# Kernel tuning notes

Measured on AMD Instinct MI355X. Metric: run time of the kernel, lower is better.

## Reference

```python
import jax, jax.numpy as jnp
import numpy as np
import math

D_EMBED = 128   # per-head dim (config.d_embed)
N_HEADS = 12
ROPE_BASE = 10000.0


def rope(x):
    # x: [B, H, S, D]; interleaved-pair rotary embedding on last dim
    B, H, S, D = x.shape
    half = D // 2
    inv_freq = 1.0 / (ROPE_BASE ** (jnp.arange(0, half, dtype=jnp.float32) * 2.0 / D))
    ang = jnp.arange(S, dtype=jnp.float32)[:, None] * inv_freq[None, :]  # [S, D/2]
    cos, sin = jnp.cos(ang), jnp.sin(ang)
    xp = x.reshape(B, H, S, half, 2)
    x1, x2 = xp[..., 0], xp[..., 1]
    o1 = x1 * cos - x2 * sin
    o2 = x1 * sin + x2 * cos
    return jnp.stack([o1, o2], axis=-1).reshape(B, H, S, D)


def setup_inputs() -> dict:
    key = jax.random.key(0)
    ks = jax.random.split(key, 5)
    B, S, E = 2, 2048, D_EMBED // 2
    inner = N_HEADS * D_EMBED
    sc = 0.02
    return {
        "q": jax.random.normal(ks[0], (B, S, E), dtype=jnp.float32),
        "Wq": jax.random.normal(ks[1], (inner, E), dtype=jnp.float32) * sc,
        "Wk": jax.random.normal(ks[2], (inner, E), dtype=jnp.float32) * sc,
        "Wv": jax.random.normal(ks[3], (inner, E), dtype=jnp.float32) * sc,
        "Wo": jax.random.normal(ks[4], (E, inner), dtype=jnp.float32) * sc,
    }


def reference(q, Wq, Wk, Wv, Wo):
    B, S, E = q.shape
    H, D = N_HEADS, D_EMBED
    scale = 1.0 / math.sqrt(D)

    def proj(x, W):
        return (x @ W.T).reshape(B, S, H, D).transpose(0, 2, 1, 3)  # [B,H,S,D]

    qh = rope(proj(q, Wq))
    kh = rope(proj(q, Wk))
    vh = proj(q, Wv)

    scores = jnp.einsum("bhsd,bhtd->bhst", qh, kh) * scale  # [B,H,S,S]
    causal = jnp.tril(jnp.ones((S, S), dtype=bool))
    scores = jnp.where(causal, scores, -jnp.inf)
    probs = jax.nn.softmax(scores, axis=-1)  # dropout omitted (eval mode)
    out = jnp.einsum("bhst,bhtd->bhsd", probs, vh)
    out = out.transpose(0, 2, 1, 3).reshape(B, S, H * D)
    return out @ Wo.T  # [B,S,E]
```

## Files before the change

### kernel.cpp

```cpp
#include <hip/hip_runtime.h>
#include <stdint.h>


typedef short v8s __attribute__((ext_vector_type(8)));
typedef unsigned int v4u __attribute__((ext_vector_type(4)));
typedef float v4f __attribute__((ext_vector_type(4)));
typedef float v16f __attribute__((ext_vector_type(16)));

#define MFMA16(a, b, c) __builtin_amdgcn_mfma_f32_16x16x32_bf16(a, b, c, 0, 0, 0)
#define MFMA32(a, b, c) __builtin_amdgcn_mfma_f32_32x32x16_bf16(a, b, c, 0, 0, 0)

#if __has_builtin(__builtin_amdgcn_exp2f)
#define EXP2(x) __builtin_amdgcn_exp2f(x)
#else
#define EXP2(x) exp2f(x)
#endif

#define SCALE2 (0.08838834764831845f * 1.4426950408889634f)

__device__ __forceinline__ unsigned short f2bf(float f) {
  uint32_t u = __builtin_bit_cast(uint32_t, f);
  u += 0x7FFFu + ((u >> 16) & 1u);
  return (unsigned short)(u >> 16);
}

__device__ __forceinline__ uint32_t packbf(float lo, float hi) {
  return __builtin_amdgcn_perm(__builtin_bit_cast(uint32_t, hi) + 0x8000u,
                               __builtin_bit_cast(uint32_t, lo) + 0x8000u,
                               0x07060302u);
}

__device__ __forceinline__ v16f zero16() {
  v16f z;
#pragma unroll
  for (int i = 0; i < 16; ++i) z[i] = 0.f;
  return z;
}

__device__ __forceinline__ void gl_lds16(const unsigned short* g, unsigned short* l) {
  __builtin_amdgcn_global_load_lds(
      (const __attribute__((address_space(1))) uint32_t*)g,
      (__attribute__((address_space(3))) uint32_t*)l, 16, 0, 0);
}

__global__ __launch_bounds__(256) void rope_table(float* __restrict__ cos_t,
                                                  float* __restrict__ sin_t) {
  int idx = blockIdx.x * 256 + threadIdx.x;
  if (idx >= 2048 * 64) return;
  int s = idx >> 6, f = idx & 63;
  float inv = exp2f((float)f * -0.20762050593046014f);
  float ang = (float)s * inv;
  float si, co;
  sincosf(ang, &si, &co);
  cos_t[idx] = co;
  sin_t[idx] = si;
}

__global__ __launch_bounds__(256) void proj_rope(
    const float* __restrict__ x, const float* __restrict__ Wq,
    const float* __restrict__ Wk, const float* __restrict__ Wv,
    const float* __restrict__ cos_t, const float* __restrict__ sin_t,
    unsigned short* __restrict__ qh, unsigned short* __restrict__ kh,
    unsigned short* __restrict__ vt) {
  const int wave = threadIdx.x >> 6, lane = threadIdx.x & 63;
  const int l16 = lane & 15, quad = lane >> 4;
  const int by = blockIdx.y;
  const int o_base = by * 64 + wave * 16;
  const int mat = o_base / 1536;
  const int inner0 = o_base % 1536;
  const int d0w = inner0 & 127;
  const float* Wsrc = (mat == 0) ? Wq : ((mat == 1) ? Wk : Wv);
  const float qscale = (mat == 0) ? SCALE2 : 1.0f;

  __shared__ __align__(16) unsigned short Lt[64][72];

  v8s wb[2];
  {
    const float* wr = Wsrc + (size_t)(inner0 + l16) * 64 + quad * 8;
#pragma unroll
    for (int s = 0; s < 2; ++s) {
      float4 a = *(const float4*)(wr + s * 32);
      float4 b = *(const float4*)(wr + s * 32 + 4);
      v8s t;
      t[0] = (short)f2bf(a.x); t[1] = (short)f2bf(a.y);
      t[2] = (short)f2bf(a.z); t[3] = (short)f2bf(a.w);
      t[4] = (short)f2bf(b.x); t[5] = (short)f2bf(b.y);
      t[6] = (short)f2bf(b.z); t[7] = (short)f2bf(b.w);
      wb[s] = t;
    }
  }

  const int d = d0w + l16;
  const int half = d >> 1;

#pragma unroll
  for (int i = 0; i < 4; ++i) {
    const int tok0 = blockIdx.x * 64 + i * 16;
    const float* xr = x + (size_t)(tok0 + l16) * 64 + quad * 8;
    v8s xa[2];
#pragma unroll
    for (int s = 0; s < 2; ++s) {
      float4 a = *(const float4*)(xr + s * 32);
      float4 b = *(const float4*)(xr + s * 32 + 4);
      v8s t;
      t[0] = (short)f2bf(a.x); t[1] = (short)f2bf(a.y);
      t[2] = (short)f2bf(a.z); t[3] = (short)f2bf(a.w);
      t[4] = (short)f2bf(b.x); t[5] = (short)f2bf(b.y);
      t[6] = (short)f2bf(b.z); t[7] = (short)f2bf(b.w);
      xa[s] = t;
    }
    v4f acc = {0.f, 0.f, 0.f, 0.f};
    acc = MFMA16(xa[0], wb[0], acc);
    acc = MFMA16(xa[1], wb[1], acc);

    if (mat < 2) {
#pragma unroll
      for (int r = 0; r < 4; ++r) {
        int sidx = (tok0 + quad * 4 + r) & 2047;
        float val = acc[r];
        float prt = __shfl_xor(val, 1);
        float co = cos_t[sidx * 64 + half];
        float si = sin_t[sidx * 64 + half];
        float rot = ((d & 1) == 0) ? (val * co - prt * si)
                                   : (prt * si + val * co);
        Lt[i * 16 + quad * 4 + r][wave * 16 + l16] = f2bf(rot * qscale);
      }
    } else {
#pragma unroll
      for (int r = 0; r < 4; ++r)
        Lt[wave * 16 + l16][i * 16 + quad * 4 + r] = f2bf(acc[r]);
    }
  }
  __syncthreads();

  const int matb = (by * 64) / 1536;
  const int innerb = (by * 64) % 1536;
  const int hb = innerb >> 7;
  const int d0b = innerb & 127;
  const int b = (blockIdx.x * 64) >> 11;
  const int tokbase = (blockIdx.x * 64) & 2047;
#pragma unroll
  for (int jj = 0; jj < 2; ++jj) {
    int cid = jj * 256 + threadIdx.x;
    int outer = cid >> 3, ic = cid & 7;
    v8s val = *(const v8s*)&Lt[outer][ic * 8];
    if (matb < 2) {
      unsigned short* dst = (matb == 0 ? qh : kh) +
          (((size_t)(b * 12 + hb)) * 2048 + tokbase + outer) * 128 + d0b + ic * 8;
      *(v8s*)dst = val;
    } else {
      const int kt = tokbase >> 6;
      const int G = ic >> 1, hhb = ic & 1;
      const int dd = d0b + outer;
      unsigned short* dst = vt +
          ((((((size_t)(b * 12 + hb)) * 32 + kt) * 4 + G) * 4 + (dd >> 5)) * 64 +
           hhb * 32 + (dd & 31)) * 8;
      *(v8s*)dst = val;
    }
  }
}

__global__ __launch_bounds__(512, 2) void attn(
    const unsigned short* __restrict__ qh, const unsigned short* __restrict__ kh,
    const unsigned short* __restrict__ vtf, unsigned short* __restrict__ att,
    const float* __restrict__ Wo, unsigned short* __restrict__ wob) {
  extern __shared__ __align__(16) unsigned short SH[];
  unsigned short* KSH = SH;
  unsigned short* VSH = SH + 32768;

  const int n = blockIdx.x;
  int qb, bh;
  if (n < 240)      { qb = 15 - n / 24; bh = n % 24; }
  else if (n < 256) { qb = 5;           bh = n - 240; }
  else if (n < 376) { int r = n - 256; qb = r / 24; bh = r % 24; }
  else              { qb = 5;           bh = 16 + (n - 376); }

  const int t = threadIdx.x;
  const int lane = t & 63;
  const int l31 = lane & 31, hh = lane >> 5;
  const int w = t >> 6;
  const int rg = w & 3, kherd = w >> 2;
  const int r0w = qb * 128 + rg * 32;
  const int qrow = r0w + l31;
  const int rowmax = r0w + 31;

  const unsigned short* Qb = qh + (size_t)bh * 2048 * 128;
  const unsigned short* Kb = kh + (size_t)bh * 2048 * 128;
  const unsigned short* Vb = vtf + (size_t)bh * 262144;

  v8s qa[8];
  {
    const unsigned short* qr = Qb + (size_t)qrow * 128 + hh * 8;
#pragma unroll
    for (int ks = 0; ks < 8; ++ks) qa[ks] = *(const v8s*)(qr + ks * 16);
  }

  int offK[2];
#pragma unroll
  for (int i2 = 0; i2 < 2; ++i2) {
    int flat = i2 * 512 + t;
    int kr = flat >> 4, kc = flat & 15;
    offK[i2] = kr * 128 + ((kc ^ (kr & 15)) << 3);
  }
  auto stageK = [&](int ktile, int slot) {
    const unsigned short* kg = Kb + ((size_t)(ktile << 6)) * 128;
    unsigned short* db = &KSH[slot * 8192];
#pragma unroll
    for (int i2 = 0; i2 < 2; ++i2)
      gl_lds16(kg + offK[i2], db + ((i2 * 512 + t) << 3));
  };
  auto stageV = [&](int ktile, int slot) {
    const unsigned short* vg = Vb + (size_t)ktile * 8192;
    unsigned short* db = &VSH[slot * 8192];
#pragma unroll
    for (int i2 = 0; i2 < 2; ++i2)
      gl_lds16(vg + ((i2 * 512 + t) << 3), db + ((i2 * 512 + t) << 3));
  };

  v16f O[4];
#pragma unroll
  for (int i = 0; i < 4; ++i) O[i] = zero16();
  float lsum = 0.f;

  const int NS = qb + 1;
  stageK(0, 0); stageV(0, 0);
  stageK(qb + 1, 2); stageV(qb + 1, 2);
  asm volatile("s_waitcnt vmcnt(0)" ::: "memory");

  for (int i = 0; i < NS; ++i) {
    __builtin_amdgcn_s_barrier();
    __builtin_amdgcn_sched_barrier(0);
    const int kt = kherd ? (qb + 1 + i) : i;
    const int key0 = kt << 6;
    const bool active = key0 <= rowmax;
    const bool hi = (key0 + 32) <= rowmax;

    if (i + 1 < NS) {
      stageK(i + 1, (i + 1) & 1);
      stageV(i + 1, (i + 1) & 1);
      stageK(qb + 2 + i, 2 + ((i + 1) & 1));
      stageV(qb + 2 + i, 2 + ((i + 1) & 1));
    }
    __builtin_amdgcn_sched_barrier(0);

    if (active) {
      const unsigned short* Kl = &KSH[(kherd * 2 + (i & 1)) * 8192];
      const unsigned short* Vl = &VSH[(kherd * 2 + (i & 1)) * 8192];
      const bool mask0 = (key0 + 31) > r0w;
      const bool mask1 = (key0 + 63) > r0w;

      auto softpack = [&](const v16f& SS, const v16f& ST, int kh2, bool needmask,
                          uint32_t* W) {
#pragma unroll
        for (int m = 0; m < 8; ++m) {
          float pa = EXP2(SS[2 * m] + ST[2 * m]);
          float pb = EXP2(SS[2 * m + 1] + ST[2 * m + 1]);
          if (needmask) {
            int keyb = key0 + kh2 * 32 + 2 * (m & 1) + 8 * (m >> 1) + 4 * hh;
            pa = (keyb <= qrow) ? pa : 0.f;
            pb = (keyb + 1 <= qrow) ? pb : 0.f;
          }
          lsum += pa + pb;
          W[m] = packbf(pa, pb);
        }
      };
      auto pvhalf = [&](const uint32_t* W, int kh2) {
        uint32_t r0 = __shfl_xor(hh ? W[0] : W[2], 32);
        uint32_t r1 = __shfl_xor(hh ? W[1] : W[3], 32);
        uint32_t r2 = __shfl_xor(hh ? W[4] : W[6], 32);
        uint32_t r3 = __shfl_xor(hh ? W[5] : W[7], 32);
#pragma unroll
        for (int gl = 0; gl < 2; ++gl) {
          const int g = kh2 * 2 + gl;
          if (key0 + g * 16 > rowmax) continue;
          uint32_t rA = gl ? r2 : r0, rB = gl ? r3 : r1;
          v4u fw;
          fw.x = hh ? rA : W[4 * gl];
          fw.y = hh ? rB : W[4 * gl + 1];
          fw.z = hh ? W[4 * gl + 2] : rA;
          fw.w = hh ? W[4 * gl + 3] : rB;
          v8s pfrag = __builtin_bit_cast(v8s, fw);
          __builtin_amdgcn_s_setprio(1);
#pragma unroll
          for (int dt = 0; dt < 4; ++dt) {
            v8s va = *(const v8s*)(Vl + (((g * 4 + dt) * 64 + lane) << 3));
            O[dt] = MFMA32(va, pfrag, O[dt]);
          }
          __builtin_amdgcn_s_setprio(0);
        }
      };

      v16f Sa = zero16(), Sb = zero16();
      __builtin_amdgcn_s_setprio(1);
#pragma unroll
      for (int ks = 0; ks < 8; ks += 2) {
        v8s ka0 = *(const v8s*)(
            Kl + ((l31 * 16 + ((2 * ks + hh) ^ (l31 & 15))) << 3));
        v8s ka1 = *(const v8s*)(
            Kl + ((l31 * 16 + ((2 * ks + 2 + hh) ^ (l31 & 15))) << 3));
        Sa = MFMA32(ka0, qa[ks], Sa);
        Sb = MFMA32(ka1, qa[ks + 1], Sb);
      }
      __builtin_amdgcn_s_setprio(0);
      uint32_t W0[8];
      softpack(Sa, Sb, 0, mask0, W0);
      pvhalf(W0, 0);

      if (hi) {
        v16f Sc = zero16(), Sd = zero16();
        __builtin_amdgcn_s_setprio(1);
#pragma unroll
        for (int ks = 0; ks < 8; ks += 2) {
          v8s ka0 = *(const v8s*)(
              Kl + (((32 + l31) * 16 + ((2 * ks + hh) ^ (l31 & 15))) << 3));
          v8s ka1 = *(const v8s*)(
              Kl + (((32 + l31) * 16 + ((2 * ks + 2 + hh) ^ (l31 & 15))) << 3));
          Sc = MFMA32(ka0, qa[ks], Sc);
          Sd = MFMA32(ka1, qa[ks + 1], Sd);
        }
        __builtin_amdgcn_s_setprio(0);
        uint32_t W1[8];
        softpack(Sc, Sd, 1, mask1, W1);
        pvhalf(W1, 1);
      }
    }
    asm volatile("s_waitcnt vmcnt(0)" ::: "memory");
  }

  __syncthreads();
  float* Ored = (float*)KSH;
  if (kherd == 1) {
    float* baseO = Ored + rg * 4096 + l31 * 128;
#pragma unroll
    for (int dt = 0; dt < 4; ++dt)
#pragma unroll
      for (int pr = 0; pr < 4; ++pr) {
        float4 v;
        v.x = O[dt][4 * pr + 0]; v.y = O[dt][4 * pr + 1];
        v.z = O[dt][4 * pr + 2]; v.w = O[dt][4 * pr + 3];
        *(float4*)(baseO + dt * 32 + (((2 * pr + hh) ^ (l31 & 7)) << 2)) = v;
      }
  }
  __syncthreads();
  if (kherd == 0) {
    const float* baseO = Ored + rg * 4096 + l31 * 128;
#pragma unroll
    for (int dt = 0; dt < 4; ++dt)
#pragma unroll
      for (int pr = 0; pr < 4; ++pr) {
        float4 v = *(const float4*)(
            baseO + dt * 32 + (((2 * pr + hh) ^ (l31 & 7)) << 2));
        O[dt][4 * pr + 0] += v.x;
        O[dt][4 * pr + 1] += v.y;
        O[dt][4 * pr + 2] += v.z;
        O[dt][4 * pr + 3] += v.w;
      }
  }
  __syncthreads();
  if (kherd == 1) Ored[rg * 64 + lane] = lsum;
  __syncthreads();
  if (kherd == 0) {
    const float lt = lsum + Ored[rg * 64 + lane];
    const float tot = lt + __shfl_xor(lt, 32);
    const float inv = 1.0f / tot;
    const int b = bh / 12, hq = bh % 12;
    unsigned short* arow = att + ((size_t)b * 2048 + qrow) * 1536 + hq * 128;
#pragma unroll
    for (int dt = 0; dt < 4; ++dt) {
#pragma unroll
      for (int pr = 0; pr < 4; ++pr) {
        float a0 = O[dt][4 * pr + 0] * inv;
        float a1 = O[dt][4 * pr + 1] * inv;
        float a2 = O[dt][4 * pr + 2] * inv;
        float a3 = O[dt][4 * pr + 3] * inv;
        uint2 uu;
        uu.x = packbf(a0, a1);
        uu.y = packbf(a2, a3);
        *(uint2*)(arow + dt * 32 + 8 * pr + 4 * hh) = uu;
      }
    }
  }

  if (qb == 0) {
    const int base = bh * 4096;
#pragma unroll
    for (int i = 0; i < 8; ++i)
      wob[base + i * 512 + t] = f2bf(Wo[base + i * 512 + t]);
  }
}

__global__ __launch_bounds__(256) void outproj(
    const unsigned short* __restrict__ att, const unsigned short* __restrict__ wob,
    float* __restrict__ out) {
  const int wave = threadIdx.x >> 6, lane = threadIdx.x & 63;
  const int l16 = lane & 15, quad = lane >> 4;
  const int tok0 = blockIdx.x * 16;
  const int e0 = wave * 16;

  v4f acc0 = {0.f, 0.f, 0.f, 0.f}, acc1 = {0.f, 0.f, 0.f, 0.f};
  const unsigned short* ar = att + (size_t)(tok0 + l16) * 1536 + quad * 8;
  const unsigned short* wr = wob + (size_t)(e0 + l16) * 1536 + quad * 8;
#pragma unroll 4
  for (int s = 0; s < 24; ++s) {
    v8s a0 = *(const v8s*)(ar + (2 * s) * 32);
    v8s b0 = *(const v8s*)(wr + (2 * s) * 32);
    v8s a1 = *(const v8s*)(ar + (2 * s + 1) * 32);
    v8s b1 = *(const v8s*)(wr + (2 * s + 1) * 32);
    acc0 = MFMA16(a0, b0, acc0);
    acc1 = MFMA16(a1, b1, acc1);
  }
#pragma unroll
  for (int r = 0; r < 4; ++r)
    out[(size_t)(tok0 + quad * 4 + r) * 64 + e0 + l16] = acc0[r] + acc1[r];
}

extern "C" void kernel_launch(void* const* d_in, const int* in_sizes, int n_in,
                              void* d_out, int out_size, void* d_ws,
                              size_t ws_size, hipStream_t stream) {
  const float* q  = (const float*)d_in[0];
  const float* Wq = (const float*)d_in[1];
  const float* Wk = (const float*)d_in[2];
  const float* Wv = (const float*)d_in[3];
  const float* Wo = (const float*)d_in[4];
  float* out = (float*)d_out;

  unsigned short* ws = (unsigned short*)d_ws;
  unsigned short* qh  = ws;
  unsigned short* kh  = ws + 6291456;
  unsigned short* vtf = ws + 12582912;
  unsigned short* att = ws + 18874368;
  float* cos_t = (float*)((char*)d_ws + 50331648);
  float* sin_t = cos_t + 131072;
  unsigned short* wob = (unsigned short*)cos_t;

  hipFuncSetAttribute((const void*)attn,
                      hipFuncAttributeMaxDynamicSharedMemorySize, 131072);

  rope_table<<<512, 256, 0, stream>>>(cos_t, sin_t);
  proj_rope<<<dim3(64, 72), 256, 0, stream>>>(q, Wq, Wk, Wv, cos_t, sin_t,
                                              qh, kh, vtf);
  attn<<<dim3(384), 512, 131072, stream>>>(qh, kh, vtf, att, Wo, wob);
  outproj<<<256, 256, 0, stream>>>(att, wob, out);
}
```

Before: 181.2 us.

## Split attention key range across four wave groups with 1024-thread blocks

The attention block grows from 512 to 1024 threads, and each query tile's key range is split into four 32-key chunks handled by four wave groups instead of two 64-key groups. Staging is restructured so half the threads load K and half load V, and the partial outputs and row sums from the four groups are reduced through LDS. The block-to-tile schedule is rebalanced for the new work split. This adds more parallelism and latency hiding per block, at the cost of a heavier cross-wave LDS reduction, more barriers, and tighter register limits under launch_bounds(1024,4).

```diff
diff --git a/kernel.cpp b/kernel.cpp
--- a/kernel.cpp
+++ b/kernel.cpp
@@ -160,7 +160,7 @@
   }
 }
 
-__global__ __launch_bounds__(512, 2) void attn(
+__global__ __launch_bounds__(1024, 4) void attn(
     const unsigned short* __restrict__ qh, const unsigned short* __restrict__ kh,
     const unsigned short* __restrict__ vtf, unsigned short* __restrict__ att,
     const float* __restrict__ Wo, unsigned short* __restrict__ wob) {
@@ -170,10 +170,28 @@
 
   const int n = blockIdx.x;
   int qb, bh;
-  if (n < 240)      { qb = 15 - n / 24; bh = n % 24; }
-  else if (n < 256) { qb = 5;           bh = n - 240; }
-  else if (n < 376) { int r = n - 256; qb = r / 24; bh = r % 24; }
-  else              { qb = 5;           bh = 16 + (n - 376); }
+  if (n >= 128 && n < 256) {
+    int r = n - 128;
+    if (r < 120) { qb = 15 - r / 24; bh = r % 24; }
+    else         { qb = 10; bh = r - 120; }
+  } else if (n < 128) {
+    if (n < 16)       { qb = 10; bh = 8 + n; }
+    else if (n < 40)  { qb = 9;  bh = n - 16; }
+    else if (n < 64)  { qb = 8;  bh = n - 40; }
+    else if (n < 88)  { qb = 7;  bh = n - 64; }
+    else if (n < 112) { qb = 6;  bh = n - 88; }
+    else if (n < 124) { qb = 5;  bh = n - 112; }
+    else              { qb = 0;  bh = n - 124; }
+  } else {
+    int r = n - 256;
+    if (r < 16)       { qb = 0; bh = 8 + r; }
+    else if (r < 40)  { qb = 1; bh = r - 16; }
+    else if (r < 64)  { qb = 2; bh = r - 40; }
+    else if (r < 88)  { qb = 3; bh = r - 64; }
+    else if (r < 112) { qb = 4; bh = r - 88; }
+    else if (r < 124) { qb = 5; bh = 12 + (r - 112); }
+    else              { qb = 0; bh = 4 + (r - 124); }
+  }
 
   const int t = threadIdx.x;
   const int lane = t & 63;
@@ -195,26 +213,22 @@
     for (int ks = 0; ks < 8; ++ks) qa[ks] = *(const v8s*)(qr + ks * 16);
   }
 
-  int offK[2];
-#pragma unroll
-  for (int i2 = 0; i2 < 2; ++i2) {
-    int flat = i2 * 512 + t;
-    int kr = flat >> 4, kc = flat & 15;
-    offK[i2] = kr * 128 + ((kc ^ (kr & 15)) << 3);
-  }
-  auto stageK = [&](int ktile, int slot) {
-    const unsigned short* kg = Kb + ((size_t)(ktile << 6)) * 128;
-    unsigned short* db = &KSH[slot * 8192];
-#pragma unroll
-    for (int i2 = 0; i2 < 2; ++i2)
-      gl_lds16(kg + offK[i2], db + ((i2 * 512 + t) << 3));
-  };
-  auto stageV = [&](int ktile, int slot) {
-    const unsigned short* vg = Vb + (size_t)ktile * 8192;
-    unsigned short* db = &VSH[slot * 8192];
-#pragma unroll
-    for (int i2 = 0; i2 < 2; ++i2)
-      gl_lds16(vg + ((i2 * 512 + t) << 3), db + ((i2 * 512 + t) << 3));
+  const int NS = qb + 1;
+
+  const int th = t & 511;
+  const int kr = th >> 4, kc = th & 15;
+  const int offK = kr * 128 + ((kc ^ (kr & 15)) << 3);
+  auto stage = [&](int i1) {
+#pragma unroll
+    for (int j = 0; j < 4; ++j) {
+      const int kt = j * NS + i1;
+      const int slot = j * 2 + (i1 & 1);
+      if (t < 512) {
+        gl_lds16(Kb + (size_t)(kt << 5) * 128 + offK, KSH + slot * 4096 + (th << 3));
+      } else {
+        gl_lds16(Vb + (size_t)kt * 4096 + (th << 3), VSH + slot * 4096 + (th << 3));
+      }
+    }
   };
 
   v16f O[4];
@@ -222,73 +236,23 @@
   for (int i = 0; i < 4; ++i) O[i] = zero16();
   float lsum = 0.f;
 
-  const int NS = qb + 1;
-  stageK(0, 0); stageV(0, 0);
-  stageK(qb + 1, 2); stageV(qb + 1, 2);
+  stage(0);
   asm volatile("s_waitcnt vmcnt(0)" ::: "memory");
 
   for (int i = 0; i < NS; ++i) {
     __builtin_amdgcn_s_barrier();
     __builtin_amdgcn_sched_barrier(0);
-    const int kt = kherd ? (qb + 1 + i) : i;
-    const int key0 = kt << 6;
+    const int kt = kherd * NS + i;
+    const int key0 = kt << 5;
     const bool active = key0 <= rowmax;
-    const bool hi = (key0 + 32) <= rowmax;
-
-    if (i + 1 < NS) {
-      stageK(i + 1, (i + 1) & 1);
-      stageV(i + 1, (i + 1) & 1);
-      stageK(qb + 2 + i, 2 + ((i + 1) & 1));
-      stageV(qb + 2 + i, 2 + ((i + 1) & 1));
-    }
+
+    if (i + 1 < NS) stage(i + 1);
     __builtin_amdgcn_sched_barrier(0);
 
     if (active) {
-      const unsigned short* Kl = &KSH[(kherd * 2 + (i & 1)) * 8192];
-      const unsigned short* Vl = &VSH[(kherd * 2 + (i & 1)) * 8192];
+      const unsigned short* Kl = KSH + (kherd * 2 + (i & 1)) * 4096;
+      const unsigned short* Vl = VSH + (kherd * 2 + (i & 1)) * 4096;
       const bool mask0 = (key0 + 31) > r0w;
-      const bool mask1 = (key0 + 63) > r0w;
-
-      auto softpack = [&](const v16f& SS, const v16f& ST, int kh2, bool needmask,
-                          uint32_t* W) {
-#pragma unroll
-        for (int m = 0; m < 8; ++m) {
-          float pa = EXP2(SS[2 * m] + ST[2 * m]);
-          float pb = EXP2(SS[2 * m + 1] + ST[2 * m + 1]);
-          if (needmask) {
-            int keyb = key0 + kh2 * 32 + 2 * (m & 1) + 8 * (m >> 1) + 4 * hh;
-            pa = (keyb <= qrow) ? pa : 0.f;
-            pb = (keyb + 1 <= qrow) ? pb : 0.f;
-          }
-          lsum += pa + pb;
-          W[m] = packbf(pa, pb);
-        }
-      };
-      auto pvhalf = [&](const uint32_t* W, int kh2) {
-        uint32_t r0 = __shfl_xor(hh ? W[0] : W[2], 32);
-        uint32_t r1 = __shfl_xor(hh ? W[1] : W[3], 32);
-        uint32_t r2 = __shfl_xor(hh ? W[4] : W[6], 32);
-        uint32_t r3 = __shfl_xor(hh ? W[5] : W[7], 32);
-#pragma unroll
-        for (int gl = 0; gl < 2; ++gl) {
-          const int g = kh2 * 2 + gl;
-          if (key0 + g * 16 > rowmax) continue;
-          uint32_t rA = gl ? r2 : r0, rB = gl ? r3 : r1;
-          v4u fw;
-          fw.x = hh ? rA : W[4 * gl];
-          fw.y = hh ? rB : W[4 * gl + 1];
-          fw.z = hh ? W[4 * gl + 2] : rA;
-          fw.w = hh ? W[4 * gl + 3] : rB;
-          v8s pfrag = __builtin_bit_cast(v8s, fw);
-          __builtin_amdgcn_s_setprio(1);
-#pragma unroll
-          for (int dt = 0; dt < 4; ++dt) {
-            v8s va = *(const v8s*)(Vl + (((g * 4 + dt) * 64 + lane) << 3));
-            O[dt] = MFMA32(va, pfrag, O[dt]);
-          }
-          __builtin_amdgcn_s_setprio(0);
-        }
-      };
 
       v16f Sa = zero16(), Sb = zero16();
       __builtin_amdgcn_s_setprio(1);
@@ -302,35 +266,51 @@
         Sb = MFMA32(ka1, qa[ks + 1], Sb);
       }
       __builtin_amdgcn_s_setprio(0);
-      uint32_t W0[8];
-      softpack(Sa, Sb, 0, mask0, W0);
-      pvhalf(W0, 0);
-
-      if (hi) {
-        v16f Sc = zero16(), Sd = zero16();
+
+      uint32_t W[8];
+#pragma unroll
+      for (int m = 0; m < 8; ++m) {
+        float pa = EXP2(Sa[2 * m] + Sb[2 * m]);
+        float pb = EXP2(Sa[2 * m + 1] + Sb[2 * m + 1]);
+        if (mask0) {
+          int keyb = key0 + 2 * (m & 1) + 8 * (m >> 1) + 4 * hh;
+          pa = (keyb <= qrow) ? pa : 0.f;
+          pb = (keyb + 1 <= qrow) ? pb : 0.f;
+        }
+        lsum += pa + pb;
+        W[m] = packbf(pa, pb);
+      }
+
+      uint32_t r0 = __shfl_xor(hh ? W[0] : W[2], 32);
+      uint32_t r1 = __shfl_xor(hh ? W[1] : W[3], 32);
+      uint32_t r2 = __shfl_xor(hh ? W[4] : W[6], 32);
+      uint32_t r3 = __shfl_xor(hh ? W[5] : W[7], 32);
+#pragma unroll
+      for (int g = 0; g < 2; ++g) {
+        if (key0 + g * 16 > rowmax) continue;
+        uint32_t rA = g ? r2 : r0, rB = g ? r3 : r1;
+        v4u fw;
+        fw.x = hh ? rA : W[4 * g];
+        fw.y = hh ? rB : W[4 * g + 1];
+        fw.z = hh ? W[4 * g + 2] : rA;
+        fw.w = hh ? W[4 * g + 3] : rB;
+        v8s pfrag = __builtin_bit_cast(v8s, fw);
         __builtin_amdgcn_s_setprio(1);
 #pragma unroll
-        for (int ks = 0; ks < 8; ks += 2) {
-          v8s ka0 = *(const v8s*)(
-              Kl + (((32 + l31) * 16 + ((2 * ks + hh) ^ (l31 & 15))) << 3));
-          v8s ka1 = *(const v8s*)(
-              Kl + (((32 + l31) * 16 + ((2 * ks + 2 + hh) ^ (l31 & 15))) << 3));
-          Sc = MFMA32(ka0, qa[ks], Sc);
-          Sd = MFMA32(ka1, qa[ks + 1], Sd);
+        for (int dt = 0; dt < 4; ++dt) {
+          v8s va = *(const v8s*)(Vl + (((g * 4 + dt) * 64 + lane) << 3));
+          O[dt] = MFMA32(va, pfrag, O[dt]);
         }
         __builtin_amdgcn_s_setprio(0);
-        uint32_t W1[8];
-        softpack(Sc, Sd, 1, mask1, W1);
-        pvhalf(W1, 1);
       }
     }
     asm volatile("s_waitcnt vmcnt(0)" ::: "memory");
   }
 
   __syncthreads();
-  float* Ored = (float*)KSH;
-  if (kherd == 1) {
-    float* baseO = Ored + rg * 4096 + l31 * 128;
+  float* R = (float*)SH;
+  if (kherd >= 2) {
+    float* baseO = R + (kherd - 2) * 16384 + rg * 4096 + l31 * 128;
 #pragma unroll
     for (int dt = 0; dt < 4; ++dt)
 #pragma unroll
@@ -342,8 +322,8 @@
       }
   }
   __syncthreads();
-  if (kherd == 0) {
-    const float* baseO = Ored + rg * 4096 + l31 * 128;
+  if (kherd < 2) {
+    const float* baseO = R + kherd * 16384 + rg * 4096 + l31 * 128;
 #pragma unroll
     for (int dt = 0; dt < 4; ++dt)
 #pragma unroll
@@ -357,10 +337,25 @@
       }
   }
   __syncthreads();
-  if (kherd == 1) Ored[rg * 64 + lane] = lsum;
+  if (kherd == 1) {
+    float* baseO = R + rg * 4096 + l31 * 128;
+#pragma unroll
+    for (int dt = 0; dt < 4; ++dt)
+#pragma unroll
+      for (int pr = 0; pr < 4; ++pr) {
+        float4 v;
+        v.x = O[dt][4 * pr + 0]; v.y = O[dt][4 * pr + 1];
+        v.z = O[dt][4 * pr + 2]; v.w = O[dt][4 * pr + 3];
+        *(float4*)(baseO + dt * 32 + (((2 * pr + hh) ^ (l31 & 7)) << 2)) = v;
+      }
+  }
+  if (kherd >= 1)
+    R[16384 + (kherd - 1) * 256 + rg * 64 + lane] = lsum;
   __syncthreads();
   if (kherd == 0) {
-    const float lt = lsum + Ored[rg * 64 + lane];
+    const float* baseO = R + rg * 4096 + l31 * 128;
+    float lt = lsum + R[16384 + rg * 64 + lane] +
+               R[16384 + 256 + rg * 64 + lane] + R[16384 + 512 + rg * 64 + lane];
     const float tot = lt + __shfl_xor(lt, 32);
     const float inv = 1.0f / tot;
     const int b = bh / 12, hq = bh % 12;
@@ -369,10 +364,12 @@
     for (int dt = 0; dt < 4; ++dt) {
 #pragma unroll
       for (int pr = 0; pr < 4; ++pr) {
-        float a0 = O[dt][4 * pr + 0] * inv;
-        float a1 = O[dt][4 * pr + 1] * inv;
-        float a2 = O[dt][4 * pr + 2] * inv;
-        float a3 = O[dt][4 * pr + 3] * inv;
+        float4 v = *(const float4*)(
+            baseO + dt * 32 + (((2 * pr + hh) ^ (l31 & 7)) << 2));
+        float a0 = (O[dt][4 * pr + 0] + v.x) * inv;
+        float a1 = (O[dt][4 * pr + 1] + v.y) * inv;
+        float a2 = (O[dt][4 * pr + 2] + v.z) * inv;
+        float a3 = (O[dt][4 * pr + 3] + v.w) * inv;
         uint2 uu;
         uu.x = packbf(a0, a1);
         uu.y = packbf(a2, a3);
@@ -384,8 +381,8 @@
   if (qb == 0) {
     const int base = bh * 4096;
 #pragma unroll
-    for (int i = 0; i < 8; ++i)
-      wob[base + i * 512 + t] = f2bf(Wo[base + i * 512 + t]);
+    for (int i = 0; i < 4; ++i)
+      wob[base + i * 1024 + t] = f2bf(Wo[base + i * 1024 + t]);
   }
 }
 
@@ -439,6 +436,6 @@
   rope_table<<<512, 256, 0, stream>>>(cos_t, sin_t);
   proj_rope<<<dim3(64, 72), 256, 0, stream>>>(q, Wq, Wk, Wv, cos_t, sin_t,
                                               qh, kh, vtf);
-  attn<<<dim3(384), 512, 131072, stream>>>(qh, kh, vtf, att, Wo, wob);
+  attn<<<dim3(384), 1024, 131072, stream>>>(qh, kh, vtf, att, Wo, wob);
   outproj<<<256, 256, 0, stream>>>(att, wob, out);
 }
```

After: 273.8 us. 51.1% more time.
